# Kernel tuning notes

Measured on AMD Instinct MI355X. Metric: run time of the kernel, lower is better.

## Reference

```python
import jax, jax.numpy as jnp
import numpy as np

B, N, D, H, P = 8, 1025, 768, 12, 32  # n = P*P + 1 (CLS + patches)
HD = D // H
EPS = 1e-5


def setup_inputs() -> dict:
    key = jax.random.key(0)
    ks = jax.random.split(key, 6)
    return {
        "x": jax.random.normal(ks[0], (B, N, D), dtype=jnp.float32),
        "canny": jax.random.uniform(ks[1], (B, 1, P, P), dtype=jnp.float32),
        "noise": jax.random.uniform(ks[2], (B, P, P), dtype=jnp.float32),
        "ln_w": jnp.ones((D,), dtype=jnp.float32),
        "ln_b": jnp.zeros((D,), dtype=jnp.float32),
        "w_qkv": (jax.random.normal(ks[3], (D, 3 * D), dtype=jnp.float32) * 0.02),
        "w_out": (jax.random.normal(ks[4], (D, D), dtype=jnp.float32) * 0.02),
        "b_out": jnp.zeros((D,), dtype=jnp.float32),
    }


def reference(x, canny, noise, ln_w, ln_b, w_qkv, w_out, b_out):
    b, n, d = x.shape
    # LayerNorm
    mu = jnp.mean(x, axis=-1, keepdims=True)
    var = jnp.mean(jnp.square(x - mu), axis=-1, keepdims=True)
    x_norm = (x - mu) * jax.lax.rsqrt(var + EPS) * ln_w + ln_b
    # QKV projection (no bias), split into heads: [b, n, 3, h, hd]
    qkv = (x_norm @ w_qkv).reshape(b, n, 3, H, HD)
    q = jnp.transpose(qkv[:, :, 0], (0, 2, 1, 3))  # [b, h, n, hd]
    k = jnp.transpose(qkv[:, :, 1], (0, 2, 1, 3))
    v = jnp.transpose(qkv[:, :, 2], (0, 2, 1, 3))
    # NOTE: source uses scale = dim ** -0.5 (full dim, not head_dim)
    dots = jnp.einsum('bhid,bhjd->bhij', q, k) * (d ** -0.5)
    # CLS-row prior injection: softmax over patch keys of CLS query row
    attn_row = jax.nn.softmax(dots[:, :, 0, 1:], axis=-1)  # [b, h, n-1]
    canny_flat = canny.reshape(b, -1) + 1.0                # [b, n-1]
    canny_flat = canny_flat / jnp.sum(canny_flat, axis=-1, keepdims=True)
    noise_flat = noise.reshape(b, -1)                      # [b, n-1]
    noise_flat = noise_flat / jnp.sum(noise_flat, axis=-1, keepdims=True)
    attn_row = attn_row + canny_flat[:, None, :] + noise_flat[:, None, :]
    dots = dots.at[:, :, 0, 1:].set(attn_row)
    # Second (full) softmax; dropout is identity in eval mode
    attn = jax.nn.softmax(dots, axis=-1)
    out = jnp.einsum('bhij,bhjd->bhid', attn, v)           # [b, h, n, hd]
    out = jnp.transpose(out, (0, 2, 1, 3)).reshape(b, n, d)
    return out @ w_out + b_out
```

## Files before the change

### kernel.cpp

```cpp
#include <hip/hip_runtime.h>

#define B_ 8
#define N_ 1025
#define D_ 768
#define H_ 12
#define NP_ 1024
#define ROWS_ (B_*N_)
#define ROWS_PAD_ 8320
#define QKVC_ 2304
#define SCALE_ 0.03608439182435161f
#define EPS_ 1e-5f

typedef float f32x4 __attribute__((ext_vector_type(4)));
typedef short s16x8 __attribute__((ext_vector_type(8)));
typedef unsigned short u16x4 __attribute__((ext_vector_type(4)));

#define GLD16(g, l) __builtin_amdgcn_global_load_lds( \
    (const __attribute__((address_space(1))) unsigned int*)(g), \
    (__attribute__((address_space(3))) unsigned int*)(l), 16, 0, 0)

__device__ __forceinline__ float blo(unsigned int u){
  union { unsigned int i; float f; } v; v.i = u << 16; return v.f;
}
__device__ __forceinline__ float bhi(unsigned int u){
  union { unsigned int i; float f; } v; v.i = u & 0xffff0000u; return v.f;
}
__device__ __forceinline__ float bf2f(unsigned short u){
  union { unsigned int i; float f; } v; v.i = ((unsigned int)u) << 16; return v.f;
}
__device__ __forceinline__ unsigned short f2bf(float f){
  union { unsigned int i; float f; } v; v.f = f;
  unsigned int b = v.i;
  b = b + 0x7fffu + ((b >> 16) & 1u);
  return (unsigned short)(b >> 16);
}
__device__ __forceinline__ unsigned int pkbf2(float a, float b){
  union { float f; unsigned int i; } ua, ub;
  ua.f = a; ub.f = b;
  return __builtin_amdgcn_perm(ub.i + 0x8000u, ua.i + 0x8000u, 0x07060302u);
}

__global__ __launch_bounds__(256) void transpose_f2b(
    const float* __restrict__ src, unsigned short* __restrict__ dst,
    int K, int N) {
  __shared__ unsigned short tile[32][33];
  int kb = blockIdx.y * 32, nb = blockIdx.x * 32;
  int tx = threadIdx.x & 31, ty = threadIdx.x >> 5;
  #pragma unroll
  for (int i = 0; i < 4; i++) {
    int r = ty + i * 8;
    tile[r][tx] = f2bf(src[(size_t)(kb + r) * N + nb + tx]);
  }
  __syncthreads();
  #pragma unroll
  for (int i = 0; i < 4; i++) {
    int r = ty + i * 8;
    dst[(size_t)(nb + r) * K + kb + tx] = tile[tx][r];
  }
}

__global__ __launch_bounds__(256) void layernorm_k(
    const float* __restrict__ x, const float* __restrict__ w,
    const float* __restrict__ b, unsigned short* __restrict__ xn) {
  int row = blockIdx.x;
  int t = threadIdx.x;
  const float* xr = x + (size_t)row * D_;
  float v0 = xr[t], v1 = xr[t + 256], v2 = xr[t + 512];
  __shared__ float rs[256], rq[256];
  rs[t] = v0 + v1 + v2;
  rq[t] = v0 * v0 + v1 * v1 + v2 * v2;
  __syncthreads();
  for (int st = 128; st > 0; st >>= 1) {
    if (t < st) { rs[t] += rs[t + st]; rq[t] += rq[t + st]; }
    __syncthreads();
  }
  float mean = rs[0] * (1.0f / 768.0f);
  float var = rq[0] * (1.0f / 768.0f) - mean * mean;
  var = var < 0.f ? 0.f : var;
  float rstd = rsqrtf(var + EPS_);
  unsigned short* yr = xn + (size_t)row * D_;
  yr[t]       = f2bf((v0 - mean) * rstd * w[t]       + b[t]);
  yr[t + 256] = f2bf((v1 - mean) * rstd * w[t + 256] + b[t + 256]);
  yr[t + 512] = f2bf((v2 - mean) * rstd * w[t + 512] + b[t + 512]);
}

template <bool OF32>
__global__ __launch_bounds__(256) void gemm_bt(
    const unsigned short* __restrict__ A, const unsigned short* __restrict__ Bt,
    void* __restrict__ Cv, const float* __restrict__ bias,
    int Mvalid, int Nn, int Kk) {
  __shared__ short sh[16384];
  short (*As)[4096] = (short (*)[4096])sh;
  short (*Bs)[4096] = (short (*)[4096])(sh + 8192);
  int t = threadIdx.x;
  int bm = blockIdx.y * 128, bn = blockIdx.x * 128;
  int lane = t & 63, wave = t >> 6;
  int wm = (wave & 1) * 64, wn = (wave >> 1) * 64;
  int m16 = lane & 15, quad = lane >> 4;
  f32x4 acc[4][4];
  #pragma unroll
  for (int i = 0; i < 4; i++)
    #pragma unroll
    for (int j = 0; j < 4; j++) acc[i][j] = (f32x4){0.f, 0.f, 0.f, 0.f};

  int e0 = t * 8;
  int e1 = (t + 256) * 8;
  int r0 = e0 >> 5, c0 = e0 & 31;
  int r1 = e1 >> 5, c1 = e1 & 31;
  const unsigned short* a0p = A + (size_t)(bm + r0) * Kk + c0;
  const unsigned short* a1p = A + (size_t)(bm + r1) * Kk + c1;
  const unsigned short* b0p = Bt + (size_t)(bn + r0) * Kk + c0;
  const unsigned short* b1p = Bt + (size_t)(bn + r1) * Kk + c1;

  int ksteps = Kk >> 6;
  for (int kt = 0; kt < ksteps; kt++) {
    int k0 = kt * 64, k1 = kt * 64 + 32;
    __syncthreads();
    GLD16(a0p + k0, &As[0][e0]);
    GLD16(a1p + k0, &As[0][e1]);
    GLD16(a0p + k1, &As[1][e0]);
    GLD16(a1p + k1, &As[1][e1]);
    GLD16(b0p + k0, &Bs[0][e0]);
    GLD16(b1p + k0, &Bs[0][e1]);
    GLD16(b0p + k1, &Bs[1][e0]);
    GLD16(b1p + k1, &Bs[1][e1]);
    __syncthreads();
    #pragma unroll
    for (int hh = 0; hh < 2; hh++) {
      s16x8 af[4], bfr[4];
      #pragma unroll
      for (int i = 0; i < 4; i++) {
        af[i]  = *(const s16x8*)(&As[hh][(wm + i * 16 + m16) * 32 + quad * 8]);
        bfr[i] = *(const s16x8*)(&Bs[hh][(wn + i * 16 + m16) * 32 + quad * 8]);
      }
      #pragma unroll
      for (int i = 0; i < 4; i++)
        #pragma unroll
        for (int j = 0; j < 4; j++)
          acc[i][j] = __builtin_amdgcn_mfma_f32_16x16x32_bf16(af[i], bfr[j], acc[i][j], 0, 0, 0);
    }
  }
  if (!OF32) {
    unsigned short* C = (unsigned short*)Cv;
    __syncthreads();
    #pragma unroll
    for (int j = 0; j < 4; j++) {
      int col = wn + j * 16 + m16;
      #pragma unroll
      for (int i = 0; i < 4; i++)
        #pragma unroll
        for (int r = 0; r < 4; r++)
          sh[(wm + i * 16 + quad * 4 + r) * 128 + col] = (short)f2bf(acc[i][j][r]);
    }
    __syncthreads();
    #pragma unroll
    for (int c = 0; c < 8; c++) {
      int idx = c * 256 + t;
      int row = idx >> 4, col = (idx & 15) * 8;
      if (bm + row < Mvalid)
        *(uint4*)(&C[(size_t)(bm + row) * Nn + bn + col]) = *(const uint4*)(&sh[row * 128 + col]);
    }
  } else {
    float* Cf = (float*)Cv;
    float* shf = (float*)sh;
    #pragma unroll
    for (int half = 0; half < 2; half++) {
      __syncthreads();
      if ((wn >> 6) == half) {
        #pragma unroll
        for (int j = 0; j < 4; j++) {
          int col_l = wn + j * 16 + m16;
          float bv = bias ? bias[bn + col_l] : 0.f;
          #pragma unroll
          for (int i = 0; i < 4; i++)
            #pragma unroll
            for (int r = 0; r < 4; r++)
              shf[(wm + i * 16 + quad * 4 + r) * 64 + (col_l & 63)] = acc[i][j][r] + bv;
        }
      }
      __syncthreads();
      #pragma unroll
      for (int c = 0; c < 8; c++) {
        int idx = c * 256 + t;
        int row = idx >> 4, col = (idx & 15) * 4;
        if (bm + row < Mvalid)
          *(float4*)(&Cf[(size_t)(bm + row) * Nn + bn + half * 64 + col]) =
              *(const float4*)(&shf[row * 64 + col]);
      }
    }
  }
}

__device__ __forceinline__ float block_sum(float v, float* red) {
  int t = threadIdx.x;
  red[t] = v;
  __syncthreads();
  for (int st = 128; st > 0; st >>= 1) {
    if (t < st) red[t] += red[t + st];
    __syncthreads();
  }
  float r = red[0];
  __syncthreads();
  return r;
}

__global__ __launch_bounds__(256) void attn_cls(
    const unsigned short* __restrict__ qkv, const float* __restrict__ canny,
    const float* __restrict__ noise, unsigned short* __restrict__ attn_out) {
  int bh = blockIdx.x;
  int b = bh / H_, h = bh % H_;
  int t = threadIdx.x;
  __shared__ float s[N_];
  __shared__ float red[256];
  __shared__ float q[64];
  __shared__ float pvred[64 * 33];

  if (t < 64) q[t] = bf2f(qkv[(size_t)(b * N_) * QKVC_ + h * 64 + t]);
  __syncthreads();

  for (int j = t; j < N_; j += 256) {
    const unsigned short* krow = qkv + (size_t)(b * N_ + j) * QKVC_ + D_ + h * 64;
    float dot = 0.f;
    #pragma unroll
    for (int c = 0; c < 8; c++) {
      uint4 kk = *(const uint4*)(krow + c * 8);
      dot += q[c*8+0]*blo(kk.x) + q[c*8+1]*bhi(kk.x)
           + q[c*8+2]*blo(kk.y) + q[c*8+3]*bhi(kk.y)
           + q[c*8+4]*blo(kk.z) + q[c*8+5]*bhi(kk.z)
           + q[c*8+6]*blo(kk.w) + q[c*8+7]*bhi(kk.w);
    }
    s[j] = dot * SCALE_;
  }
  float cp = 0.f, npp = 0.f;
  for (int j = t; j < NP_; j += 256) {
    cp  += canny[b * NP_ + j] + 1.0f;
    npp += noise[b * NP_ + j];
  }
  float csum = block_sum(cp, red);
  float nsum = block_sum(npp, red);
  float e1 = 0.f;
  for (int j = t; j < N_; j += 256) if (j >= 1) e1 += __expf(s[j]);
  float sum1 = block_sum(e1, red);
  for (int j = t; j < N_; j += 256) {
    if (j >= 1) {
      s[j] = __expf(s[j]) / sum1
           + (canny[b * NP_ + j - 1] + 1.0f) / csum
           + noise[b * NP_ + j - 1] / nsum;
    }
  }
  __syncthreads();
  float e2 = 0.f;
  for (int j = t; j < N_; j += 256) { float e = __expf(s[j]); s[j] = e; e2 += e; }
  float sum2 = block_sum(e2, red);
  {
    int o = t & 7, g = t >> 3;
    float a[8] = {0.f, 0.f, 0.f, 0.f, 0.f, 0.f, 0.f, 0.f};
    for (int j = g; j < N_; j += 32) {
      float sv = s[j];
      uint4 vv = *(const uint4*)(qkv + (size_t)(b * N_ + j) * QKVC_ + 2 * D_ + h * 64 + o * 8);
      a[0] += sv * blo(vv.x); a[1] += sv * bhi(vv.x);
      a[2] += sv * blo(vv.y); a[3] += sv * bhi(vv.y);
      a[4] += sv * blo(vv.z); a[5] += sv * bhi(vv.z);
      a[6] += sv * blo(vv.w); a[7] += sv * bhi(vv.w);
    }
    #pragma unroll
    for (int i = 0; i < 8; i++) pvred[(o * 8 + i) * 33 + g] = a[i];
  }
  __syncthreads();
  if (t < 64) {
    float acc = 0.f;
    #pragma unroll
    for (int u = 0; u < 32; u++) acc += pvred[t * 33 + u];
    attn_out[(size_t)(b * N_) * D_ + h * 64 + t] = f2bf(acc / sum2);
  }
}

__global__ __launch_bounds__(256) void attn_main(
    const unsigned short* __restrict__ qkv, unsigned short* __restrict__ attn_out) {
  int id = blockIdx.x;
  int tile = id / 96;
  int rem = id % 96;
  int h = rem >> 3;
  int b = rem & 7;
  int t = threadIdx.x;
  int lane = t & 63, w = t >> 6;
  int m16 = lane & 15, quad = lane >> 4;

  __shared__ short ps[128 * 72];
  __shared__ short ks[64 * 72];
  __shared__ unsigned int vs[64 * 36];
  __shared__ float lsum[128];
  __shared__ float tailbuf[256];

  int qbase = 1 + tile * 128;

  {
    int r = t >> 1, seg = (t & 1) * 32;
    const uint4* src = (const uint4*)(qkv + (size_t)(b * N_ + qbase + r) * QKVC_ + h * 64 + seg);
    uint4 u0 = src[0], u1 = src[1], u2 = src[2], u3 = src[3];
    *(uint4*)(&ps[r * 72 + seg])      = u0;
    *(uint4*)(&ps[r * 72 + seg + 8])  = u1;
    *(uint4*)(&ps[r * 72 + seg + 16]) = u2;
    *(uint4*)(&ps[r * 72 + seg + 24]) = u3;
  }
  s16x8 qb[2][2];
  #pragma unroll
  for (int nt = 0; nt < 2; nt++)
    #pragma unroll
    for (int ks_ = 0; ks_ < 2; ks_++)
      qb[nt][ks_] = *(const s16x8*)(&ps[(w * 32 + nt * 16 + m16) * 72 + ks_ * 32 + quad * 8]);

  f32x4 oacc[2][4];
  #pragma unroll
  for (int mt = 0; mt < 2; mt++)
    #pragma unroll
    for (int dt = 0; dt < 4; dt++) oacc[mt][dt] = (f32x4){0.f, 0.f, 0.f, 0.f};
  float lp[2] = {0.f, 0.f};

  for (int jt = 0; jt < 16; jt++) {
    __syncthreads();
    {
      int key = t >> 2, seg = (t & 3) * 16;
      int j = jt * 64 + key;
      const uint4* src = (const uint4*)(qkv + (size_t)(b * N_ + j) * QKVC_ + D_ + h * 64 + seg);
      uint4 k0 = src[0], k1 = src[1];
      *(uint4*)(&ks[key * 72 + seg])     = k0;
      *(uint4*)(&ks[key * 72 + seg + 8]) = k1;
    }
    {
      int p2 = t & 31, seg = t >> 5;
      int j0 = jt * 64 + 2 * p2, j1 = j0 + 1;
      uint4 va = *(const uint4*)(qkv + (size_t)(b * N_ + j0) * QKVC_ + 2 * D_ + h * 64 + seg * 8);
      uint4 vb = *(const uint4*)(qkv + (size_t)(b * N_ + j1) * QKVC_ + 2 * D_ + h * 64 + seg * 8);
      const unsigned int* vaw = (const unsigned int*)&va;
      const unsigned int* vbw = (const unsigned int*)&vb;
      #pragma unroll
      for (int i = 0; i < 4; i++) {
        vs[(seg * 8 + 2 * i)     * 36 + p2] = __builtin_amdgcn_perm(vbw[i], vaw[i], 0x05040100u);
        vs[(seg * 8 + 2 * i + 1) * 36 + p2] = __builtin_amdgcn_perm(vbw[i], vaw[i], 0x07060302u);
      }
    }
    __syncthreads();
    f32x4 sacc[4][2];
    #pragma unroll
    for (int kt = 0; kt < 4; kt++) {
      s16x8 ka0 = *(const s16x8*)(&ks[(kt * 16 + m16) * 72 + quad * 8]);
      s16x8 ka1 = *(const s16x8*)(&ks[(kt * 16 + m16) * 72 + 32 + quad * 8]);
      #pragma unroll
      for (int nt = 0; nt < 2; nt++) {
        f32x4 s = (f32x4){0.f, 0.f, 0.f, 0.f};
        s = __builtin_amdgcn_mfma_f32_16x16x32_bf16(ka0, qb[nt][0], s, 0, 0, 0);
        s = __builtin_amdgcn_mfma_f32_16x16x32_bf16(ka1, qb[nt][1], s, 0, 0, 0);
        sacc[kt][nt] = s;
      }
    }
    #pragma unroll
    for (int kt = 0; kt < 4; kt++) {
      #pragma unroll
      for (int nt = 0; nt < 2; nt++) {
        f32x4 s = sacc[kt][nt];
        float p0 = __expf(s[0] * SCALE_);
        float p1 = __expf(s[1] * SCALE_);
        float p2 = __expf(s[2] * SCALE_);
        float p3 = __expf(s[3] * SCALE_);
        lp[nt] += p0 + p1 + p2 + p3;
        uint2 pk = {pkbf2(p0, p1), pkbf2(p2, p3)};
        *(uint2*)(&ps[(w * 32 + nt * 16 + m16) * 72 + kt * 16 + quad * 4]) = pk;
      }
    }
    __syncthreads();
    s16x8 pa[2][2];
    #pragma unroll
    for (int mt = 0; mt < 2; mt++)
      #pragma unroll
      for (int ks_ = 0; ks_ < 2; ks_++)
        pa[mt][ks_] = *(const s16x8*)(&ps[(w * 32 + mt * 16 + m16) * 72 + ks_ * 32 + quad * 8]);
    const short* vss = (const short*)vs;
    #pragma unroll
    for (int dt = 0; dt < 4; dt++) {
      s16x8 vb0 = *(const s16x8*)(&vss[(dt * 16 + m16) * 72 + quad * 8]);
      s16x8 vb1 = *(const s16x8*)(&vss[(dt * 16 + m16) * 72 + 32 + quad * 8]);
      #pragma unroll
      for (int mt = 0; mt < 2; mt++) {
        oacc[mt][dt] = __builtin_amdgcn_mfma_f32_16x16x32_bf16(pa[mt][0], vb0, oacc[mt][dt], 0, 0, 0);
        oacc[mt][dt] = __builtin_amdgcn_mfma_f32_16x16x32_bf16(pa[mt][1], vb1, oacc[mt][dt], 0, 0, 0);
      }
    }
  }
  if (t < 64)       tailbuf[t]      = bf2f(qkv[(size_t)(b * N_ + 1024) * QKVC_ + D_     + h * 64 + t]);
  else if (t < 128) tailbuf[64 + (t - 64)] = bf2f(qkv[(size_t)(b * N_ + 1024) * QKVC_ + 2 * D_ + h * 64 + (t - 64)]);
  __syncthreads();
  #pragma unroll
  for (int nt = 0; nt < 2; nt++) {
    float d = 0.f;
    #pragma unroll
    for (int jj = 0; jj < 8; jj++) {
      d += bf2f((unsigned short)qb[nt][0][jj]) * tailbuf[quad * 8 + jj];
      d += bf2f((unsigned short)qb[nt][1][jj]) * tailbuf[32 + quad * 8 + jj];
    }
    d += __shfl_xor(d, 16, 64);
    d += __shfl_xor(d, 32, 64);
    float p = __expf(d * SCALE_);
    lp[nt] += p * 0.25f;
    if (quad == 0) tailbuf[128 + w * 32 + nt * 16 + m16] = p;
  }
  __syncthreads();
  #pragma unroll
  for (int mt = 0; mt < 2; mt++)
    #pragma unroll
    for (int r = 0; r < 4; r++) {
      float pr = tailbuf[128 + w * 32 + mt * 16 + quad * 4 + r];
      #pragma unroll
      for (int dt = 0; dt < 4; dt++)
        oacc[mt][dt][r] += pr * tailbuf[64 + dt * 16 + m16];
    }
  #pragma unroll
  for (int nt = 0; nt < 2; nt++) {
    float l = lp[nt];
    l += __shfl_xor(l, 16, 64);
    l += __shfl_xor(l, 32, 64);
    if (quad == 0) lsum[w * 32 + nt * 16 + m16] = l;
  }
  __syncthreads();
  #pragma unroll
  for (int mt = 0; mt < 2; mt++) {
    float rinv[4];
    #pragma unroll
    for (int r = 0; r < 4; r++) rinv[r] = 1.0f / lsum[w * 32 + mt * 16 + quad * 4 + r];
    #pragma unroll
    for (int dt = 0; dt < 4; dt++) {
      #pragma unroll
      for (int r = 0; r < 4; r++) {
        int grow = b * N_ + qbase + w * 32 + mt * 16 + quad * 4 + r;
        attn_out[(size_t)grow * D_ + h * 64 + dt * 16 + m16] = f2bf(oacc[mt][dt][r] * rinv[r]);
      }
    }
  }
}

extern "C" void kernel_launch(void* const* d_in, const int* in_sizes, int n_in,
                              void* d_out, int out_size, void* d_ws, size_t ws_size,
                              hipStream_t stream) {
  (void)in_sizes; (void)n_in; (void)out_size; (void)ws_size;
  const float* x     = (const float*)d_in[0];
  const float* canny = (const float*)d_in[1];
  const float* noise = (const float*)d_in[2];
  const float* lnw   = (const float*)d_in[3];
  const float* lnb   = (const float*)d_in[4];
  const float* wqkv  = (const float*)d_in[5];
  const float* wout  = (const float*)d_in[6];
  const float* bout  = (const float*)d_in[7];
  float* out = (float*)d_out;
  char* ws = (char*)d_ws;

  unsigned short* xn    = (unsigned short*)(ws);
  unsigned short* wqkvT = (unsigned short*)(ws + 12779520);
  unsigned short* woutT = (unsigned short*)(ws + 16318464);
  unsigned short* qkv   = (unsigned short*)(ws + 17498112);

  transpose_f2b<<<dim3(QKVC_ / 32, D_ / 32), 256, 0, stream>>>(wqkv, wqkvT, D_, QKVC_);
  transpose_f2b<<<dim3(D_ / 32, D_ / 32), 256, 0, stream>>>(wout, woutT, D_, D_);
  layernorm_k<<<dim3(ROWS_), 256, 0, stream>>>(x, lnw, lnb, xn);
  gemm_bt<false><<<dim3(QKVC_ / 128, ROWS_PAD_ / 128), 256, 0, stream>>>(
      xn, wqkvT, (void*)qkv, nullptr, ROWS_, QKVC_, D_);
  attn_cls<<<dim3(B_ * H_), 256, 0, stream>>>(qkv, canny, noise, xn);
  attn_main<<<dim3(8 * H_ * B_), 256, 0, stream>>>(qkv, xn);
  gemm_bt<true><<<dim3(D_ / 128, ROWS_PAD_ / 128), 256, 0, stream>>>(
      xn, woutT, (void*)out, bout, ROWS_, D_, D_);
}
```

Baseline: 236.8 us.

## Prefetch K/V into registers, fold scale into Q, MFMA row sums, merge transposes

```diff
diff --git a/kernel.cpp b/kernel.cpp
--- a/kernel.cpp
+++ b/kernel.cpp
@@ -13,7 +13,6 @@
 
 typedef float f32x4 __attribute__((ext_vector_type(4)));
 typedef short s16x8 __attribute__((ext_vector_type(8)));
-typedef unsigned short u16x4 __attribute__((ext_vector_type(4)));
 
 #define GLD16(g, l) __builtin_amdgcn_global_load_lds( \
     (const __attribute__((address_space(1))) unsigned int*)(g), \
@@ -40,11 +39,15 @@
   return __builtin_amdgcn_perm(ub.i + 0x8000u, ua.i + 0x8000u, 0x07060302u);
 }
 
-__global__ __launch_bounds__(256) void transpose_f2b(
-    const float* __restrict__ src, unsigned short* __restrict__ dst,
-    int K, int N) {
+__global__ __launch_bounds__(256) void transpose_f2b2(
+    const float* __restrict__ w1, unsigned short* __restrict__ d1,
+    const float* __restrict__ w2, unsigned short* __restrict__ d2) {
   __shared__ unsigned short tile[32][33];
-  int kb = blockIdx.y * 32, nb = blockIdx.x * 32;
+  int bx = blockIdx.x;
+  const float* src; unsigned short* dst; int N, nb;
+  if (bx < 72) { src = w1; dst = d1; N = QKVC_; nb = bx * 32; }
+  else         { src = w2; dst = d2; N = D_;    nb = (bx - 72) * 32; }
+  int kb = blockIdx.y * 32;
   int tx = threadIdx.x & 31, ty = threadIdx.x >> 5;
   #pragma unroll
   for (int i = 0; i < 4; i++) {
@@ -55,7 +58,7 @@
   #pragma unroll
   for (int i = 0; i < 4; i++) {
     int r = ty + i * 8;
-    dst[(size_t)(nb + r) * K + kb + tx] = tile[tx][r];
+    dst[(size_t)(nb + r) * D_ + kb + tx] = tile[tx][r];
   }
 }
 
@@ -66,16 +69,21 @@
   int t = threadIdx.x;
   const float* xr = x + (size_t)row * D_;
   float v0 = xr[t], v1 = xr[t + 256], v2 = xr[t + 512];
-  __shared__ float rs[256], rq[256];
-  rs[t] = v0 + v1 + v2;
-  rq[t] = v0 * v0 + v1 * v1 + v2 * v2;
-  __syncthreads();
-  for (int st = 128; st > 0; st >>= 1) {
-    if (t < st) { rs[t] += rs[t + st]; rq[t] += rq[t + st]; }
-    __syncthreads();
-  }
-  float mean = rs[0] * (1.0f / 768.0f);
-  float var = rq[0] * (1.0f / 768.0f) - mean * mean;
+  float s = v0 + v1 + v2;
+  float q = v0 * v0 + v1 * v1 + v2 * v2;
+  #pragma unroll
+  for (int off = 32; off > 0; off >>= 1) {
+    s += __shfl_xor(s, off, 64);
+    q += __shfl_xor(q, off, 64);
+  }
+  __shared__ float r8[8];
+  int wv = t >> 6;
+  if ((t & 63) == 0) { r8[wv] = s; r8[4 + wv] = q; }
+  __syncthreads();
+  s = r8[0] + r8[1] + r8[2] + r8[3];
+  q = r8[4] + r8[5] + r8[6] + r8[7];
+  float mean = s * (1.0f / 768.0f);
+  float var = q * (1.0f / 768.0f) - mean * mean;
   var = var < 0.f ? 0.f : var;
   float rstd = rsqrtf(var + EPS_);
   unsigned short* yr = xn + (size_t)row * D_;
@@ -289,7 +297,6 @@
   __shared__ short ps[128 * 72];
   __shared__ short ks[64 * 72];
   __shared__ unsigned int vs[64 * 36];
-  __shared__ float lsum[128];
   __shared__ float tailbuf[256];
 
   int qbase = 1 + tile * 128;
@@ -307,40 +314,58 @@
   #pragma unroll
   for (int nt = 0; nt < 2; nt++)
     #pragma unroll
-    for (int ks_ = 0; ks_ < 2; ks_++)
+    for (int ks_ = 0; ks_ < 2; ks_++) {
       qb[nt][ks_] = *(const s16x8*)(&ps[(w * 32 + nt * 16 + m16) * 72 + ks_ * 32 + quad * 8]);
-
-  f32x4 oacc[2][4];
-  #pragma unroll
-  for (int mt = 0; mt < 2; mt++)
+      unsigned int* u = (unsigned int*)&qb[nt][ks_];
+      #pragma unroll
+      for (int i = 0; i < 4; i++)
+        u[i] = pkbf2(blo(u[i]) * SCALE_, bhi(u[i]) * SCALE_);
+    }
+  s16x8 vone;
+  #pragma unroll
+  for (int i = 0; i < 8; i++) vone[i] = (short)0x3F80;
+
+  f32x4 oacc[2][4], lacc[2];
+  #pragma unroll
+  for (int mt = 0; mt < 2; mt++) {
+    lacc[mt] = (f32x4){0.f, 0.f, 0.f, 0.f};
     #pragma unroll
     for (int dt = 0; dt < 4; dt++) oacc[mt][dt] = (f32x4){0.f, 0.f, 0.f, 0.f};
-  float lp[2] = {0.f, 0.f};
+  }
+
+  int kkey = t >> 2, kseg = (t & 3) * 16;
+  const unsigned short* kbase = qkv + (size_t)(b * N_) * QKVC_ + D_ + h * 64;
+  int vp2 = t & 31, vseg = t >> 5;
+  const unsigned short* vbase = qkv + (size_t)(b * N_) * QKVC_ + 2 * D_ + h * 64 + vseg * 8;
+  uint4 kr0, kr1, vr0, vr1;
+  {
+    const uint4* ksrc = (const uint4*)(kbase + (size_t)kkey * QKVC_ + kseg);
+    kr0 = ksrc[0]; kr1 = ksrc[1];
+    vr0 = *(const uint4*)(vbase + (size_t)(2 * vp2) * QKVC_);
+    vr1 = *(const uint4*)(vbase + (size_t)(2 * vp2 + 1) * QKVC_);
+  }
 
   for (int jt = 0; jt < 16; jt++) {
     __syncthreads();
+    *(uint4*)(&ks[kkey * 72 + kseg])     = kr0;
+    *(uint4*)(&ks[kkey * 72 + kseg + 8]) = kr1;
     {
-      int key = t >> 2, seg = (t & 3) * 16;
-      int j = jt * 64 + key;
-      const uint4* src = (const uint4*)(qkv + (size_t)(b * N_ + j) * QKVC_ + D_ + h * 64 + seg);
-      uint4 k0 = src[0], k1 = src[1];
-      *(uint4*)(&ks[key * 72 + seg])     = k0;
-      *(uint4*)(&ks[key * 72 + seg + 8]) = k1;
-    }
-    {
-      int p2 = t & 31, seg = t >> 5;
-      int j0 = jt * 64 + 2 * p2, j1 = j0 + 1;
-      uint4 va = *(const uint4*)(qkv + (size_t)(b * N_ + j0) * QKVC_ + 2 * D_ + h * 64 + seg * 8);
-      uint4 vb = *(const uint4*)(qkv + (size_t)(b * N_ + j1) * QKVC_ + 2 * D_ + h * 64 + seg * 8);
-      const unsigned int* vaw = (const unsigned int*)&va;
-      const unsigned int* vbw = (const unsigned int*)&vb;
+      const unsigned int* vaw = (const unsigned int*)&vr0;
+      const unsigned int* vbw = (const unsigned int*)&vr1;
       #pragma unroll
       for (int i = 0; i < 4; i++) {
-        vs[(seg * 8 + 2 * i)     * 36 + p2] = __builtin_amdgcn_perm(vbw[i], vaw[i], 0x05040100u);
-        vs[(seg * 8 + 2 * i + 1) * 36 + p2] = __builtin_amdgcn_perm(vbw[i], vaw[i], 0x07060302u);
-      }
-    }
-    __syncthreads();
+        vs[(vseg * 8 + 2 * i)     * 36 + vp2] = __builtin_amdgcn_perm(vbw[i], vaw[i], 0x05040100u);
+        vs[(vseg * 8 + 2 * i + 1) * 36 + vp2] = __builtin_amdgcn_perm(vbw[i], vaw[i], 0x07060302u);
+      }
+    }
+    __syncthreads();
+    if (jt < 15) {
+      int j0 = (jt + 1) * 64;
+      const uint4* ksrc = (const uint4*)(kbase + (size_t)(j0 + kkey) * QKVC_ + kseg);
+      kr0 = ksrc[0]; kr1 = ksrc[1];
+      vr0 = *(const uint4*)(vbase + (size_t)(j0 + 2 * vp2) * QKVC_);
+      vr1 = *(const uint4*)(vbase + (size_t)(j0 + 2 * vp2 + 1) * QKVC_);
+    }
     f32x4 sacc[4][2];
     #pragma unroll
     for (int kt = 0; kt < 4; kt++) {
@@ -359,11 +384,10 @@
       #pragma unroll
       for (int nt = 0; nt < 2; nt++) {
         f32x4 s = sacc[kt][nt];
-        float p0 = __expf(s[0] * SCALE_);
-        float p1 = __expf(s[1] * SCALE_);
-        float p2 = __expf(s[2] * SCALE_);
-        float p3 = __expf(s[3] * SCALE_);
-        lp[nt] += p0 + p1 + p2 + p3;
+        float p0 = __expf(s[0]);
+        float p1 = __expf(s[1]);
+        float p2 = __expf(s[2]);
+        float p3 = __expf(s[3]);
         uint2 pk = {pkbf2(p0, p1), pkbf2(p2, p3)};
         *(uint2*)(&ps[(w * 32 + nt * 16 + m16) * 72 + kt * 16 + quad * 4]) = pk;
       }
@@ -386,8 +410,13 @@
         oacc[mt][dt] = __builtin_amdgcn_mfma_f32_16x16x32_bf16(pa[mt][1], vb1, oacc[mt][dt], 0, 0, 0);
       }
     }
-  }
-  if (t < 64)       tailbuf[t]      = bf2f(qkv[(size_t)(b * N_ + 1024) * QKVC_ + D_     + h * 64 + t]);
+    #pragma unroll
+    for (int mt = 0; mt < 2; mt++) {
+      lacc[mt] = __builtin_amdgcn_mfma_f32_16x16x32_bf16(pa[mt][0], vone, lacc[mt], 0, 0, 0);
+      lacc[mt] = __builtin_amdgcn_mfma_f32_16x16x32_bf16(pa[mt][1], vone, lacc[mt], 0, 0, 0);
+    }
+  }
+  if (t < 64)       tailbuf[t]             = bf2f(qkv[(size_t)(b * N_ + 1024) * QKVC_ + D_     + h * 64 + t]);
   else if (t < 128) tailbuf[64 + (t - 64)] = bf2f(qkv[(size_t)(b * N_ + 1024) * QKVC_ + 2 * D_ + h * 64 + (t - 64)]);
   __syncthreads();
   #pragma unroll
@@ -400,8 +429,7 @@
     }
     d += __shfl_xor(d, 16, 64);
     d += __shfl_xor(d, 32, 64);
-    float p = __expf(d * SCALE_);
-    lp[nt] += p * 0.25f;
+    float p = __expf(d);
     if (quad == 0) tailbuf[128 + w * 32 + nt * 16 + m16] = p;
   }
   __syncthreads();
@@ -410,23 +438,16 @@
     #pragma unroll
     for (int r = 0; r < 4; r++) {
       float pr = tailbuf[128 + w * 32 + mt * 16 + quad * 4 + r];
+      lacc[mt][r] += pr;
       #pragma unroll
       for (int dt = 0; dt < 4; dt++)
         oacc[mt][dt][r] += pr * tailbuf[64 + dt * 16 + m16];
     }
   #pragma unroll
-  for (int nt = 0; nt < 2; nt++) {
-    float l = lp[nt];
-    l += __shfl_xor(l, 16, 64);
-    l += __shfl_xor(l, 32, 64);
-    if (quad == 0) lsum[w * 32 + nt * 16 + m16] = l;
-  }
-  __syncthreads();
-  #pragma unroll
   for (int mt = 0; mt < 2; mt++) {
     float rinv[4];
     #pragma unroll
-    for (int r = 0; r < 4; r++) rinv[r] = 1.0f / lsum[w * 32 + mt * 16 + quad * 4 + r];
+    for (int r = 0; r < 4; r++) rinv[r] = 1.0f / lacc[mt][r];
     #pragma unroll
     for (int dt = 0; dt < 4; dt++) {
       #pragma unroll
@@ -458,8 +479,7 @@
   unsigned short* woutT = (unsigned short*)(ws + 16318464);
   unsigned short* qkv   = (unsigned short*)(ws + 17498112);
 
-  transpose_f2b<<<dim3(QKVC_ / 32, D_ / 32), 256, 0, stream>>>(wqkv, wqkvT, D_, QKVC_);
-  transpose_f2b<<<dim3(D_ / 32, D_ / 32), 256, 0, stream>>>(wout, woutT, D_, D_);
+  transpose_f2b2<<<dim3(96, 24), 256, 0, stream>>>(wqkv, wqkvT, wout, woutT);
   layernorm_k<<<dim3(ROWS_), 256, 0, stream>>>(x, lnw, lnb, xn);
   gemm_bt<false><<<dim3(QKVC_ / 128, ROWS_PAD_ / 128), 256, 0, stream>>>(
       xn, wqkvT, (void*)qkv, nullptr, ROWS_, QKVC_, D_);
```

Result: faster. 224.7 us (-5.1%).
